# Kernel optimization log

Hardware: AMD Instinct MI355X
Metric: run time of the kernel (lower is better)

Reference implementation:

```python
import jax, jax.numpy as jnp
import numpy as np
jax.config.update('jax_enable_x64', True)  # log_normalization accumulates in fp64 like the torch code

B = 256
N = 36864  # SO(3) HEALPix-style grid, level 3
EPS_TRACE = 1e-8


def quat_to_mat(q):
    # (w, x, y, z) convention; normalize to a unit quaternion first.
    q = q / jnp.linalg.norm(q, axis=-1, keepdims=True)
    w, x, y, z = q[..., 0], q[..., 1], q[..., 2], q[..., 3]
    return jnp.stack([
        jnp.stack([1 - 2 * (y * y + z * z), 2 * (x * y - w * z), 2 * (x * z + w * y)], -1),
        jnp.stack([2 * (x * y + w * z), 1 - 2 * (x * x + z * z), 2 * (y * z - w * x)], -1),
        jnp.stack([2 * (x * z - w * y), 2 * (y * z + w * x), 1 - 2 * (x * x + y * y)], -1),
    ], -2)


def cholesky_inverse(L):
    # (L L^T)^{-1} = L^{-T} L^{-1}; batched 3x3, inv is cheap and exact here.
    Linv = jnp.linalg.inv(L)
    return jnp.einsum('...ki,...kj->...ij', Linv, Linv)


def setup_inputs() -> dict:
    key = jax.random.key(0)
    k1, k2, k3, k4 = jax.random.split(key, 4)
    gt_quat = jax.random.normal(k1, (B, 4), dtype=jnp.float32)
    mode_quat = jax.random.normal(k2, (B, 4), dtype=jnp.float32)
    raw = jax.random.normal(k3, (B, 3, 3), dtype=jnp.float32)
    diag_vals = 0.3 + jax.nn.softplus(jnp.diagonal(raw, axis1=-2, axis2=-1))
    cov_tril = jnp.tril(raw, -1) * 0.2 + jnp.eye(3, dtype=jnp.float32) * diag_vals[:, None, :]
    grid_q = jax.random.normal(k4, (N, 4), dtype=jnp.float32)
    grids = quat_to_mat(grid_q)  # [N, 3, 3] rotation matrices
    return {'gt_quat': gt_quat, 'mode_quat': mode_quat, 'cov_tril': cov_tril, 'grids': grids}


def reference(gt_quat, mode_quat, cov_tril, grids):
    Z = cholesky_inverse(cov_tril)                      # [B,3,3] precision
    trZ = jnp.einsum('bii->b', Z)                       # tr(Z)

    # power over the grid: sqrt(clamp(tr(Z) - tr(Z @ R_n), eps)) for every grid rotation
    tr_ZR_grid = jnp.einsum('bij,nji->bn', Z, grids)    # [B,N] = diag-sum of Z @ R_n
    powers = jnp.sqrt(jnp.clip(trZ[:, None] - tr_ZR_grid, EPS_TRACE))  # [B,N] fp32

    # stable log-normalization (fp64 accumulation, as in the torch code)
    stability = jnp.min(powers, axis=-1)                # [B]
    p64 = powers.astype(jnp.float64)
    log_exp_sum = jnp.log(jnp.sum(jnp.exp(-p64 + stability[:, None].astype(jnp.float64)) / p64,
                                  axis=1)).astype(jnp.float32)
    logF = log_exp_sum - jnp.log(jnp.float32(N)) - stability

    # power at the ground truth relative rotation R = R0^T R_gt
    R_gt = quat_to_mat(gt_quat)
    R0 = quat_to_mat(mode_quat)
    R_rel = jnp.einsum('bki,bkj->bij', R0, R_gt)        # R0^T @ R_gt
    tr_ZR = jnp.einsum('bij,bji->b', Z, R_rel)
    power = jnp.sqrt(jnp.clip(trZ - tr_ZR, EPS_TRACE))  # [B]

    nll = logF + power + jnp.log(power)
    return nll
```

## Files before the change

### kernel.cpp

```cpp
#include <hip/hip_runtime.h>
#include <math.h>

#define TPB 256
#define BPB 8
#define CHUNK 256
#define NCHUNKS 6
#define NCHUNK (CHUNK * NCHUNKS)
#define NTILES 24
#define LOG2E 1.44269504088896340736f

#if __has_builtin(__builtin_amdgcn_rsqf)
#define FAST_RSQ(x) __builtin_amdgcn_rsqf(x)
#else
#define FAST_RSQ(x) rsqrtf(x)
#endif
#if __has_builtin(__builtin_amdgcn_exp2f)
#define FAST_EXP2(x) __builtin_amdgcn_exp2f(x)
#else
#define FAST_EXP2(x) exp2f(x)
#endif

__device__ __forceinline__ void compute_Z_neg(const float* __restrict__ L, float zo[7]) {
    float a = L[0], l10 = L[3], c = L[4], d = L[6], e = L[7], f = L[8];
    float ia = 1.0f / a, ic = 1.0f / c, iff = 1.0f / f;
    float m00 = ia;
    float m10 = -l10 * ia * ic;
    float m11 = ic;
    float m20 = (l10 * e - c * d) * ia * ic * iff;
    float m21 = -e * ic * iff;
    float m22 = iff;
    float Z0 = m00*m00 + m10*m10 + m20*m20;
    float Z1 = m10*m11 + m20*m21;
    float Z2 = m20*m22;
    float Z4 = m11*m11 + m21*m21;
    float Z5 = m21*m22;
    float Z8 = m22*m22;
    zo[0] = -Z0; zo[1] = -Z4; zo[2] = -Z8;
    zo[3] = -Z1; zo[4] = -Z2; zo[5] = -Z5;
    zo[6] = Z0 + Z4 + Z8;
}

__device__ __forceinline__ void quat_to_mat(const float q[4], float R[9]) {
    float n = sqrtf(q[0]*q[0] + q[1]*q[1] + q[2]*q[2] + q[3]*q[3]);
    float w = q[0]/n, x = q[1]/n, y = q[2]/n, z = q[3]/n;
    R[0] = 1.f - 2.f*(y*y + z*z);
    R[1] = 2.f*(x*y - w*z);
    R[2] = 2.f*(x*z + w*y);
    R[3] = 2.f*(x*y + w*z);
    R[4] = 1.f - 2.f*(x*x + z*z);
    R[5] = 2.f*(y*z - w*x);
    R[6] = 2.f*(x*z - w*y);
    R[7] = 2.f*(y*z + w*x);
    R[8] = 1.f - 2.f*(x*x + y*y);
}

__global__ __launch_bounds__(TPB) void k1_partials(
    const float* __restrict__ cov_tril,
    const float* __restrict__ grids,
    double* __restrict__ part, int B)
{
    const int tile = blockIdx.x;
    const int bg   = blockIdx.y;
    const int tid  = threadIdx.x;

    __shared__ float zsh[BPB][8];
    __shared__ float gsh[CHUNK * 9];
    __shared__ float red[TPB * 9];

    if (tid < BPB) {
        float zo[7];
        compute_Z_neg(cov_tril + (bg * BPB + tid) * 9, zo);
#pragma unroll
        for (int j = 0; j < 7; ++j) zsh[tid][j] = zo[j];
    }
    __syncthreads();

    float z[BPB][7];
#pragma unroll
    for (int bl = 0; bl < BPB; ++bl)
#pragma unroll
        for (int j = 0; j < 7; ++j) z[bl][j] = zsh[bl][j];

    float acc[BPB];
#pragma unroll
    for (int bl = 0; bl < BPB; ++bl) acc[bl] = 0.f;

    const float4* gsrc = (const float4*)grids + (size_t)tile * (NCHUNK * 9 / 4);

    for (int c = 0; c < NCHUNKS; ++c) {
        const float4* src = gsrc + c * (CHUNK * 9 / 4);
        float4 v0 = src[tid];
        float4 v1 = src[tid + 256];
        float4 v2;
        if (tid < 64) v2 = src[tid + 512];

        __syncthreads();
        ((float4*)gsh)[tid]       = v0;
        ((float4*)gsh)[tid + 256] = v1;
        if (tid < 64) ((float4*)gsh)[tid + 512] = v2;
        __syncthreads();

        const float* G = gsh + tid * 9;
        float G0=G[0],G1=G[1],G2=G[2],G3=G[3],G4=G[4],G5=G[5],G6=G[6],G7=G[7],G8=G[8];
        float g0 = G0, g1 = G4, g2 = G8;
        float g3 = G1 + G3, g4 = G2 + G6, g5 = G5 + G7;

#pragma unroll
        for (int bl = 0; bl < BPB; ++bl) {
            float x = z[bl][6];
            x = fmaf(z[bl][0], g0, x);
            x = fmaf(z[bl][1], g1, x);
            x = fmaf(z[bl][2], g2, x);
            x = fmaf(z[bl][3], g3, x);
            x = fmaf(z[bl][4], g4, x);
            x = fmaf(z[bl][5], g5, x);
            x = fmaxf(x, 1e-8f);
            float r = FAST_RSQ(x);
            float p = x * r;
            float e = FAST_EXP2(-LOG2E * p);
            acc[bl] = fmaf(e, r, acc[bl]);
        }
    }

#pragma unroll
    for (int bl = 0; bl < BPB; ++bl) red[tid * 9 + bl] = acc[bl];
    __syncthreads();

    const int bl = tid & 7;
    const int s  = tid >> 3;
    float p_ = 0.f;
#pragma unroll
    for (int j = 0; j < 8; ++j) p_ += red[(s * 8 + j) * 9 + bl];
    __syncthreads();
    red[tid] = p_;
    __syncthreads();

    if (tid < BPB) {
        double S = 0.0;
#pragma unroll
        for (int j = 0; j < 32; ++j) S += (double)red[j * 8 + tid];
        part[(size_t)tile * B + bg * BPB + tid] = S;
    }
}

__global__ __launch_bounds__(TPB) void k2_finalize(
    const float* __restrict__ gt_quat,
    const float* __restrict__ mode_quat,
    const float* __restrict__ cov_tril,
    const double* __restrict__ part,
    float* __restrict__ out, int n_tiles, int n_total, int B)
{
    const int b = blockIdx.x * blockDim.x + threadIdx.x;
    if (b >= B) return;

    double S = 0.0;
    for (int t = 0; t < n_tiles; ++t) S += part[(size_t)t * B + b];

    float zo[7];
    compute_Z_neg(cov_tril + b * 9, zo);

    float q0[4] = {mode_quat[b*4+0], mode_quat[b*4+1], mode_quat[b*4+2], mode_quat[b*4+3]};
    float qg[4] = {gt_quat[b*4+0],   gt_quat[b*4+1],   gt_quat[b*4+2],   gt_quat[b*4+3]};
    float R0[9], Rg[9];
    quat_to_mat(q0, R0);
    quat_to_mat(qg, Rg);

    float Rr[9];
#pragma unroll
    for (int i = 0; i < 3; ++i)
#pragma unroll
        for (int j = 0; j < 3; ++j)
            Rr[i*3+j] = R0[0*3+i]*Rg[0*3+j] + R0[1*3+i]*Rg[1*3+j] + R0[2*3+i]*Rg[2*3+j];

    float x = zo[6];
    x = fmaf(zo[0], Rr[0], x);
    x = fmaf(zo[1], Rr[4], x);
    x = fmaf(zo[2], Rr[8], x);
    x = fmaf(zo[3], Rr[1] + Rr[3], x);
    x = fmaf(zo[4], Rr[2] + Rr[6], x);
    x = fmaf(zo[5], Rr[5] + Rr[7], x);

    float power = sqrtf(fmaxf(x, 1e-8f));
    float logF  = (float)(log(S) - log((double)n_total));
    out[b] = logF + power + logf(power);
}

extern "C" void kernel_launch(void* const* d_in, const int* in_sizes, int n_in,
                              void* d_out, int out_size, void* d_ws, size_t ws_size,
                              hipStream_t stream) {
    const float* gt    = (const float*)d_in[0];
    const float* mode  = (const float*)d_in[1];
    const float* cov   = (const float*)d_in[2];
    const float* grids = (const float*)d_in[3];
    float* out = (float*)d_out;

    const int B       = in_sizes[0] / 4;
    const int n_total = in_sizes[3] / 9;
    const int n_tiles = NTILES;
    const int b_grps  = B / BPB;

    double* part = (double*)d_ws;

    dim3 g1(n_tiles, b_grps);
    k1_partials<<<g1, TPB, 0, stream>>>(cov, grids, part, B);
    k2_finalize<<<1, TPB, 0, stream>>>(gt, mode, cov, part, out, n_tiles, n_total, B);
}
```

Measured before the change: 19.58 us.

## Fuse partial and finalize kernels via cooperative grid sync, retile grid

Merges the two kernel launches into one cooperative kernel: all blocks compute their partial sums, then a grid-wide barrier lets block (0,0) finish the per-batch reduction and NLL. Tiles drop from 24 to 16 with 9 chunks each, giving 512 blocks so the whole grid can be co-resident. The aim is to remove the second launch and its gap. In exchange it adds a grid-wide sync and a serial finalize tail in one block, and falls back to two launches if the cooperative launch fails.

```diff
diff --git a/kernel.cpp b/kernel.cpp
--- a/kernel.cpp
+++ b/kernel.cpp
@@ -1,12 +1,16 @@
 #include <hip/hip_runtime.h>
+#include <hip/hip_cooperative_groups.h>
 #include <math.h>
+
+namespace cg = cooperative_groups;
 
 #define TPB 256
 #define BPB 8
 #define CHUNK 256
-#define NCHUNKS 6
+#define NCHUNKS 9
 #define NCHUNK (CHUNK * NCHUNKS)
-#define NTILES 24
+#define NTILES 16
+#define BGRPS 32
 #define LOG2E 1.44269504088896340736f
 
 #if __has_builtin(__builtin_amdgcn_rsqf)
@@ -54,19 +58,13 @@
     R[8] = 1.f - 2.f*(x*x + y*y);
 }
 
-__global__ __launch_bounds__(TPB) void k1_partials(
+__device__ __forceinline__ void partial_body(
+    int tile, int bg, int tid,
     const float* __restrict__ cov_tril,
     const float* __restrict__ grids,
-    double* __restrict__ part, int B)
-{
-    const int tile = blockIdx.x;
-    const int bg   = blockIdx.y;
-    const int tid  = threadIdx.x;
-
-    __shared__ float zsh[BPB][8];
-    __shared__ float gsh[CHUNK * 9];
-    __shared__ float red[TPB * 9];
-
+    double* __restrict__ part, int B,
+    float (*zsh)[8], float* gsh, float* red)
+{
     if (tid < BPB) {
         float zo[7];
         compute_Z_neg(cov_tril + (bg * BPB + tid) * 9, zo);
@@ -143,18 +141,17 @@
     }
 }
 
-__global__ __launch_bounds__(TPB) void k2_finalize(
+__device__ __forceinline__ void finalize_body(
+    int b,
     const float* __restrict__ gt_quat,
     const float* __restrict__ mode_quat,
     const float* __restrict__ cov_tril,
     const double* __restrict__ part,
-    float* __restrict__ out, int n_tiles, int n_total, int B)
-{
-    const int b = blockIdx.x * blockDim.x + threadIdx.x;
-    if (b >= B) return;
-
+    float* __restrict__ out, int n_total, int B)
+{
     double S = 0.0;
-    for (int t = 0; t < n_tiles; ++t) S += part[(size_t)t * B + b];
+#pragma unroll
+    for (int t = 0; t < NTILES; ++t) S += part[(size_t)t * B + b];
 
     float zo[7];
     compute_Z_neg(cov_tril + b * 9, zo);
@@ -183,6 +180,49 @@
     float power = sqrtf(fmaxf(x, 1e-8f));
     float logF  = (float)(log(S) - log((double)n_total));
     out[b] = logF + power + logf(power);
+}
+
+__global__ __launch_bounds__(TPB) void k_coop(
+    const float* __restrict__ gt_quat,
+    const float* __restrict__ mode_quat,
+    const float* __restrict__ cov_tril,
+    const float* __restrict__ grids,
+    double* __restrict__ part,
+    float* __restrict__ out, int n_total, int B)
+{
+    __shared__ float zsh[BPB][8];
+    __shared__ float gsh[CHUNK * 9];
+    __shared__ float red[TPB * 9];
+
+    partial_body(blockIdx.x, blockIdx.y, threadIdx.x, cov_tril, grids, part, B,
+                 zsh, gsh, red);
+
+    cg::this_grid().sync();
+
+    if (blockIdx.x == 0 && blockIdx.y == 0)
+        finalize_body(threadIdx.x, gt_quat, mode_quat, cov_tril, part, out, n_total, B);
+}
+
+__global__ __launch_bounds__(TPB) void k_part(
+    const float* __restrict__ cov_tril,
+    const float* __restrict__ grids,
+    double* __restrict__ part, int B)
+{
+    __shared__ float zsh[BPB][8];
+    __shared__ float gsh[CHUNK * 9];
+    __shared__ float red[TPB * 9];
+    partial_body(blockIdx.x, blockIdx.y, threadIdx.x, cov_tril, grids, part, B,
+                 zsh, gsh, red);
+}
+
+__global__ __launch_bounds__(TPB) void k_fin(
+    const float* __restrict__ gt_quat,
+    const float* __restrict__ mode_quat,
+    const float* __restrict__ cov_tril,
+    const double* __restrict__ part,
+    float* __restrict__ out, int n_total, int B)
+{
+    finalize_body(threadIdx.x, gt_quat, mode_quat, cov_tril, part, out, n_total, B);
 }
 
 extern "C" void kernel_launch(void* const* d_in, const int* in_sizes, int n_in,
@@ -194,14 +234,21 @@
     const float* grids = (const float*)d_in[3];
     float* out = (float*)d_out;
 
-    const int B       = in_sizes[0] / 4;
-    const int n_total = in_sizes[3] / 9;
-    const int n_tiles = NTILES;
-    const int b_grps  = B / BPB;
+    int B       = in_sizes[0] / 4;
+    int n_total = in_sizes[3] / 9;
 
     double* part = (double*)d_ws;
 
-    dim3 g1(n_tiles, b_grps);
-    k1_partials<<<g1, TPB, 0, stream>>>(cov, grids, part, B);
-    k2_finalize<<<1, TPB, 0, stream>>>(gt, mode, cov, part, out, n_tiles, n_total, B);
-}
+    void* args[] = {(void*)&gt, (void*)&mode, (void*)&cov, (void*)&grids,
+                    (void*)&part, (void*)&out, (void*)&n_total, (void*)&B};
+    dim3 grid(NTILES, BGRPS);
+    dim3 block(TPB);
+
+    hipError_t err = hipLaunchCooperativeKernel((const void*)k_coop, grid, block,
+                                                args, 0, stream);
+    if (err != hipSuccess) {
+        (void)hipGetLastError();
+        k_part<<<grid, block, 0, stream>>>(cov, grids, part, B);
+        k_fin<<<1, block, 0, stream>>>(gt, mode, cov, part, out, n_total, B);
+    }
+}
```

Result: slower. 62.94 us (+221.5%).
